# Performance work log

Hardware: AMD Instinct MI355X
Metric: run time of the kernel (lower is better)

## Reference

```python
import jax, jax.numpy as jnp
import numpy as np

E = 768            # bert_embed_dim
D = 3 * E          # LSTM input size = bert_embed_dim * 3
H = 3 * E          # LSTM hidden size = bert_embed_dim * 3
B = 16             # batch
T = 64             # max sequence length


def setup_inputs() -> dict:
    key = jax.random.key(0)
    ks = jax.random.split(key, 12)
    mention_feature = jax.random.normal(ks[0], (B, T, D), jnp.float32)
    start = jax.random.randint(ks[1], (B,), 1, T // 2).astype(jnp.int32)
    end = (start + jax.random.randint(ks[2], (B,), 1, 8)).astype(jnp.int32)
    length = jnp.minimum(end + jax.random.randint(ks[3], (B,), 0, T // 2), T)
    mention_mask = (jnp.arange(T)[None, :] < length[:, None]).astype(jnp.int32)
    s = 0.02
    W_ih = jax.random.normal(ks[4], (4 * H, D), jnp.float32) * s
    W_hh = jax.random.normal(ks[5], (4 * H, H), jnp.float32) * s
    b_ih = jax.random.normal(ks[6], (4 * H,), jnp.float32) * s
    b_hh = jax.random.normal(ks[7], (4 * H,), jnp.float32) * s
    W_out = jax.random.normal(ks[8], (E, 2 * H), jnp.float32) * s
    b_out = jax.random.normal(ks[9], (E,), jnp.float32) * s
    return dict(mention_feature=mention_feature, mention_mask=mention_mask,
                start=start, end=end, W_ih=W_ih, W_hh=W_hh, b_ih=b_ih,
                b_hh=b_hh, W_out=W_out, b_out=b_out)


def lstm_last(seq, lens, W_ih, W_hh, b_ih, b_hh):
    """Masked single-layer LSTM over padded [B,T,D] seqs; returns last valid h [B,H].
    PyTorch gate order: i, f, g, o. State frozen once t >= lens, so the final
    carry equals the output at each sample's last valid timestep."""
    Bb, Tt, _ = seq.shape
    Hh = W_hh.shape[1]
    # precompute input projection for all steps: [B,T,4H]
    xp = jnp.einsum('btd,gd->btg', seq, W_ih) + (b_ih + b_hh)

    def step(carry, inp):
        h, c = carry
        xt, t = inp
        gates = xt + h @ W_hh.T  # [B,4H]
        i_, f_, g_, o_ = jnp.split(gates, 4, axis=-1)
        c_new = jax.nn.sigmoid(f_) * c + jax.nn.sigmoid(i_) * jnp.tanh(g_)
        h_new = jax.nn.sigmoid(o_) * jnp.tanh(c_new)
        upd = (t < lens)[:, None]
        return (jnp.where(upd, h_new, h), jnp.where(upd, c_new, c)), None

    h0 = jnp.zeros((Bb, Hh), seq.dtype)
    (h, _), _ = jax.lax.scan(step, (h0, h0),
                             (xp.transpose(1, 0, 2), jnp.arange(Tt)))
    return h


def reference(mention_feature, mention_mask, start, end,
              W_ih, W_hh, b_ih, b_hh, W_out, b_out):
    Bb, Tt, Dd = mention_feature.shape
    length = jnp.sum(mention_mask, axis=-1)  # [B]

    # left context: tokens [1 : start); if start <= 1 -> single zero step
    left_seq = mention_feature[:, 1:, :]                       # [B,T-1,D]
    tl = jnp.arange(Tt - 1)
    left_valid = tl[None, :] < (start - 1)[:, None]            # [B,T-1]
    left_seq = left_seq * left_valid[..., None]
    left_len = jnp.maximum(start - 1, 1)
    h_left = lstm_last(left_seq, left_len, W_ih, W_hh, b_ih, b_hh)

    # right context: tokens [end : length); if length <= end -> single zero step
    tr = jnp.arange(Tt)
    idx = jnp.clip(end[:, None] + tr[None, :], 0, Tt - 1)      # [B,T]
    right_seq = jnp.take_along_axis(mention_feature, idx[..., None], axis=1)
    right_valid = tr[None, :] < (length - end)[:, None]
    right_seq = right_seq * right_valid[..., None]
    right_len = jnp.maximum(length - end, 1)
    h_right = lstm_last(right_seq, right_len, W_ih, W_hh, b_ih, b_hh)

    feat = jnp.concatenate([h_left, h_right], axis=-1)         # [B,6E]
    return feat @ W_out.T + b_out                              # [B,E]
```

## Files before the change

### kernel.cpp

```cpp
#include <hip/hip_runtime.h>

#define Dd 2304
#define Hh 2304
#define G4 9216
#define TMAX 32
#define NSEQ 32
#define NBLK 192

typedef __bf16 bf16x8 __attribute__((ext_vector_type(8)));
typedef float f32x4 __attribute__((ext_vector_type(4)));
typedef unsigned short u16x8 __attribute__((ext_vector_type(8)));

#define XP_OFF   16384ull
#define WIHB_OFF (XP_OFF  + 1024ull * 9216ull * 4ull)
#define ABF_OFF  (WIHB_OFF + 9216ull * 2304ull * 2ull)
#define HB_OFF   (ABF_OFF + 1024ull * 2304ull * 2ull)
#define FLAG_BASE 2560

static __device__ __forceinline__ unsigned short f2bf(float f) {
  unsigned int u = __float_as_uint(f);
  u += 0x7fffu + ((u >> 16) & 1u);
  return (unsigned short)(u >> 16);
}
static __device__ __forceinline__ float bf2f(unsigned short u) {
  return __uint_as_float(((unsigned int)u) << 16);
}
static __device__ __forceinline__ float sigm(float x) { return 1.0f / (1.0f + expf(-x)); }

static __device__ __forceinline__ void st_h_llc(unsigned short* p, unsigned short v) {
  asm volatile("global_store_short %0, %1, off sc0 sc1"
               :: "v"(p), "v"((unsigned)v) : "memory");
}

__global__ void prep_kernel(const int* __restrict__ mask, const int* __restrict__ start,
                            const int* __restrict__ endp, int* __restrict__ meta) {
  __shared__ int len_s[16];
  const int tid = threadIdx.x;
  for (int i = 2112 + tid; i < 4096; i += 256)
    meta[i] = 0;
  if (tid < 16) {
    int s = 0;
    #pragma unroll 8
    for (int t = 0; t < 64; ++t) s += mask[tid * 64 + t];
    len_s[tid] = s;
  }
  __syncthreads();
  if (tid == 0) {
    int lens[NSEQ]; int ml = 0;
    for (int s = 0; s < NSEQ; ++s) {
      int l;
      if (s < 16) l = start[s] - 1;
      else        l = len_s[s - 16] - endp[s - 16];
      if (l < 1) l = 1;
      if (l > TMAX) l = TMAX;
      lens[s] = l; meta[s] = l; if (l > ml) ml = l;
    }
    meta[32] = ml;
    int* rsrc = meta + 64;
    int* rdst = meta + 64 + 1024;
    int R = 0;
    for (int s = 0; s < NSEQ; ++s) {
      const int b = s & 15;
      const int st = start[b], ln = len_s[b], en = endp[b];
      for (int t = 0; t < lens[s]; ++t) {
        int src = -1;
        if (s < 16) { if (t < st - 1)  src = (b * 64 + t + 1) * Dd; }
        else        { if (t < ln - en) src = (b * 64 + en + t) * Dd; }
        rsrc[R] = src; rdst[R] = s * TMAX + t; ++R;
      }
    }
    meta[33] = R;
    int i = R;
    for (int s = 0; s < NSEQ; ++s)
      for (int t = lens[s]; t < TMAX; ++t) { rsrc[i] = -1; rdst[i] = s * TMAX + t; ++i; }
  }
}

__global__ void cast_wih_kernel(const float4* __restrict__ in, uint2* __restrict__ out) {
  const int i = blockIdx.x * 256 + threadIdx.x;
  const float4 v = in[i];
  uint2 o;
  o.x = (unsigned)f2bf(v.x) | ((unsigned)f2bf(v.y) << 16);
  o.y = (unsigned)f2bf(v.z) | ((unsigned)f2bf(v.w) << 16);
  out[i] = o;
}

__global__ void cast_a_kernel(const float* __restrict__ feat, const int* __restrict__ meta,
                              uint4* __restrict__ abf) {
  const int r = blockIdx.x;
  const int src = meta[64 + r];
  const int tid = threadIdx.x;
  uint4* orow = abf + (size_t)r * 288;
  for (int c = tid; c < 288; c += 256) {
    uint4 o = {0, 0, 0, 0};
    if (src >= 0) {
      const float4 f0 = *(const float4*)(feat + src + c * 8);
      const float4 f1 = *(const float4*)(feat + src + c * 8 + 4);
      o.x = (unsigned)f2bf(f0.x) | ((unsigned)f2bf(f0.y) << 16);
      o.y = (unsigned)f2bf(f0.z) | ((unsigned)f2bf(f0.w) << 16);
      o.z = (unsigned)f2bf(f1.x) | ((unsigned)f2bf(f1.y) << 16);
      o.w = (unsigned)f2bf(f1.z) | ((unsigned)f2bf(f1.w) << 16);
    }
    orow[c] = o;
  }
}

#define LDA 40
__global__ __launch_bounds__(256) void xp_gemm(
    const unsigned short* __restrict__ abf, const unsigned short* __restrict__ wihb,
    const float* __restrict__ bih, const float* __restrict__ bhh,
    const int* __restrict__ meta, float* __restrict__ xp)
{
  const int R = meta[33];
  const int m0 = blockIdx.y * 128;
  if (m0 >= R) return;
  const int n0 = blockIdx.x * 128;
  __shared__ unsigned short As[128 * LDA];
  __shared__ unsigned short Bs[128 * LDA];
  const int tid = threadIdx.x;
  const int srow = tid >> 1;
  const int skk  = (tid & 1) * 16;
  const int* rdst = meta + 64 + 1024;
  const unsigned short* ap = abf  + (size_t)(m0 + srow) * Dd + skk;
  const unsigned short* bp = wihb + (size_t)(n0 + srow) * Dd + skk;

  const int w = tid >> 6, lane = tid & 63;
  const int l16 = lane & 15, quad = lane >> 4;
  const int wm = (w >> 1) * 64, wn = (w & 1) * 64;

  f32x4 acc[4][4] = {};
  for (int kk = 0; kk < Dd; kk += 32) {
    const u16x8 a0 = *(const u16x8*)(ap + kk);
    const u16x8 a1 = *(const u16x8*)(ap + kk + 8);
    const u16x8 b0 = *(const u16x8*)(bp + kk);
    const u16x8 b1 = *(const u16x8*)(bp + kk + 8);
    __syncthreads();
    *(u16x8*)&As[srow * LDA + skk]     = a0;
    *(u16x8*)&As[srow * LDA + skk + 8] = a1;
    *(u16x8*)&Bs[srow * LDA + skk]     = b0;
    *(u16x8*)&Bs[srow * LDA + skk + 8] = b1;
    __syncthreads();
    bf16x8 af[4], bfr[4];
    #pragma unroll
    for (int i = 0; i < 4; ++i) {
      af[i]  = __builtin_bit_cast(bf16x8, *(const u16x8*)&As[(wm + i * 16 + l16) * LDA + quad * 8]);
      bfr[i] = __builtin_bit_cast(bf16x8, *(const u16x8*)&Bs[(wn + i * 16 + l16) * LDA + quad * 8]);
    }
    #pragma unroll
    for (int mi = 0; mi < 4; ++mi)
      #pragma unroll
      for (int ni = 0; ni < 4; ++ni)
        acc[mi][ni] = __builtin_amdgcn_mfma_f32_16x16x32_bf16(af[mi], bfr[ni], acc[mi][ni], 0, 0, 0);
  }
  #pragma unroll
  for (int ni = 0; ni < 4; ++ni) {
    const int col = n0 + wn + ni * 16 + l16;
    const float bsum = bih[col] + bhh[col];
    #pragma unroll
    for (int mi = 0; mi < 4; ++mi)
      #pragma unroll
      for (int r = 0; r < 4; ++r) {
        const int row = m0 + wm + mi * 16 + quad * 4 + r;
        const int dr = rdst[row];
        xp[(size_t)dr * G4 + col] = acc[mi][ni][r] + bsum;
      }
  }
}

__global__ __launch_bounds__(256, 1) void lstm_persist(
    const float* __restrict__ whh, const float* __restrict__ xp,
    int* __restrict__ meta, unsigned short* __restrict__ hb,
    const float* __restrict__ wout, const float* __restrict__ bout,
    float* __restrict__ out)
{
  const int tid = threadIdx.x;
  const int bid = blockIdx.x;
  const int j0 = bid * 12;
  const int w = tid >> 6, lane = tid & 63;
  const int l16 = lane & 15, quad = lane >> 4;
  const int maxlen = meta[32];
  int* flags = meta + FLAG_BASE;
#define HBUF(t) (hb + (size_t)(t) * (NSEQ * Hh))

  __shared__ float red[4][32][49];

  u16x8 Bfr[54];
  #pragma unroll
  for (int n = 0; n < 3; ++n) {
    const int rl = n * 16 + l16;
    const int g = rl / 12, j = rl - g * 12;
    const float* bp = whh + (size_t)(g * Hh + j0 + j) * Hh + w * 576 + quad * 8;
    #pragma unroll
    for (int kf = 0; kf < 18; ++kf) {
      const float4 f0 = *(const float4*)(bp + kf * 32);
      const float4 f1 = *(const float4*)(bp + kf * 32 + 4);
      u16x8 v;
      v[0] = f2bf(f0.x); v[1] = f2bf(f0.y); v[2] = f2bf(f0.z); v[3] = f2bf(f0.w);
      v[4] = f2bf(f1.x); v[5] = f2bf(f1.y); v[6] = f2bf(f1.z); v[7] = f2bf(f1.w);
      Bfr[n * 18 + kf] = v;
    }
  }

  const int sA = tid / 12, jA = tid - sA * 12;
  const int cB = 256 + tid;
  const int sB = cB / 12, jB = cB - sB * 12;
  const int lenA = meta[sA];
  const int lenB = (tid < 128) ? meta[sB] : 0;
  float cstA = 0.f, hvA = 0.f, cstB = 0.f, hvB = 0.f;

  {
    const float* p = xp + (size_t)(sA * TMAX) * G4 + j0 + jA;
    const float vi = p[0], vg = p[2 * Hh], vo = p[3 * Hh];
    cstA = sigm(vi) * tanhf(vg);
    hvA = sigm(vo) * tanhf(cstA);
    st_h_llc(HBUF(1) + sA * Hh + j0 + jA, f2bf(hvA));
    if (tid < 128) {
      const float* q = xp + (size_t)(sB * TMAX) * G4 + j0 + jB;
      const float wi = q[0], wg = q[2 * Hh], wo = q[3 * Hh];
      cstB = sigm(wi) * tanhf(wg);
      hvB = sigm(wo) * tanhf(cstB);
      st_h_llc(HBUF(1) + sB * Hh + j0 + jB, f2bf(hvB));
    }
  }

  float xiA, xfA, xgA, xoA, xiB = 0, xfB = 0, xgB = 0, xoB = 0;
  asm volatile("s_waitcnt vmcnt(0)" ::: "memory");
  __syncthreads();
  if (tid == 0)
    __hip_atomic_store(flags + bid, 1, __ATOMIC_RELAXED, __HIP_MEMORY_SCOPE_AGENT);
  if (1 < maxlen) {
    { const float* p = xp + (size_t)(sA * TMAX + 1) * G4 + j0 + jA;
      xiA = p[0]; xfA = p[Hh]; xgA = p[2 * Hh]; xoA = p[3 * Hh]; }
    if (tid < 128) {
      const float* q = xp + (size_t)(sB * TMAX + 1) * G4 + j0 + jB;
      xiB = q[0]; xfB = q[Hh]; xgB = q[2 * Hh]; xoB = q[3 * Hh];
    }
  }
  if (tid < NBLK) {
    while (__hip_atomic_load(flags + tid, __ATOMIC_RELAXED, __HIP_MEMORY_SCOPE_AGENT) < 1)
      __builtin_amdgcn_s_sleep(2);
  }
  __syncthreads();

  for (int t = 1; t < maxlen; ++t) {
    const unsigned short* hin = HBUF(t);
    unsigned short* hout      = HBUF(t + 1);
    f32x4 acc[2][3] = {};
    const unsigned short* pa = hin + (size_t)l16 * Hh + w * 576 + quad * 8;
    #pragma unroll
    for (int kf = 0; kf < 18; ++kf) {
      const bf16x8 a0 = __builtin_bit_cast(bf16x8, *(const u16x8*)(pa + kf * 32));
      const bf16x8 a1 = __builtin_bit_cast(bf16x8, *(const u16x8*)(pa + kf * 32 + 16 * Hh));
      #pragma unroll
      for (int n = 0; n < 3; ++n) {
        const bf16x8 bv = __builtin_bit_cast(bf16x8, Bfr[n * 18 + kf]);
        acc[0][n] = __builtin_amdgcn_mfma_f32_16x16x32_bf16(a0, bv, acc[0][n], 0, 0, 0);
        acc[1][n] = __builtin_amdgcn_mfma_f32_16x16x32_bf16(a1, bv, acc[1][n], 0, 0, 0);
      }
    }
    #pragma unroll
    for (int m = 0; m < 2; ++m)
      #pragma unroll
      for (int n = 0; n < 3; ++n)
        #pragma unroll
        for (int r = 0; r < 4; ++r)
          red[w][m * 16 + quad * 4 + r][n * 16 + l16] = acc[m][n][r];
    __syncthreads();
    if (t < lenA) {
      const float vi = xiA + red[0][sA][jA]      + red[1][sA][jA]      + red[2][sA][jA]      + red[3][sA][jA];
      const float vf = xfA + red[0][sA][12 + jA] + red[1][sA][12 + jA] + red[2][sA][12 + jA] + red[3][sA][12 + jA];
      const float vg = xgA + red[0][sA][24 + jA] + red[1][sA][24 + jA] + red[2][sA][24 + jA] + red[3][sA][24 + jA];
      const float vo = xoA + red[0][sA][36 + jA] + red[1][sA][36 + jA] + red[2][sA][36 + jA] + red[3][sA][36 + jA];
      cstA = sigm(vf) * cstA + sigm(vi) * tanhf(vg);
      hvA = sigm(vo) * tanhf(cstA);
    }
    st_h_llc(hout + sA * Hh + j0 + jA, f2bf(hvA));
    if (tid < 128) {
      if (t < lenB) {
        const float vi = xiB + red[0][sB][jB]      + red[1][sB][jB]      + red[2][sB][jB]      + red[3][sB][jB];
        const float vf = xfB + red[0][sB][12 + jB] + red[1][sB][12 + jB] + red[2][sB][12 + jB] + red[3][sB][12 + jB];
        const float vg = xgB + red[0][sB][24 + jB] + red[1][sB][24 + jB] + red[2][sB][24 + jB] + red[3][sB][24 + jB];
        const float vo = xoB + red[0][sB][36 + jB] + red[1][sB][36 + jB] + red[2][sB][36 + jB] + red[3][sB][36 + jB];
        cstB = sigm(vf) * cstB + sigm(vi) * tanhf(vg);
        hvB = sigm(vo) * tanhf(cstB);
      }
      st_h_llc(hout + sB * Hh + j0 + jB, f2bf(hvB));
    }
    asm volatile("s_waitcnt vmcnt(0)" ::: "memory");
    __syncthreads();
    if (tid == 0)
      __hip_atomic_store(flags + bid, t + 1, __ATOMIC_RELAXED, __HIP_MEMORY_SCOPE_AGENT);
    if (t + 1 < maxlen) {
      { const float* p = xp + (size_t)(sA * TMAX + t + 1) * G4 + j0 + jA;
        xiA = p[0]; xfA = p[Hh]; xgA = p[2 * Hh]; xoA = p[3 * Hh]; }
      if (tid < 128) {
        const float* q = xp + (size_t)(sB * TMAX + t + 1) * G4 + j0 + jB;
        xiB = q[0]; xfB = q[Hh]; xgB = q[2 * Hh]; xoB = q[3 * Hh];
      }
    }
    if (tid < NBLK) {
      while (__hip_atomic_load(flags + tid, __ATOMIC_RELAXED, __HIP_MEMORY_SCOPE_AGENT) < t + 1)
        __builtin_amdgcn_s_sleep(2);
    }
    __syncthreads();
  }

  const unsigned short* hf = HBUF(maxlen);
  const int o = tid >> 2, p4 = tid & 3;
  const int ee = o & 3, bb = o >> 2;
  const int e = bid * 4 + ee;
  const int hrow = (p4 < 2) ? bb : (16 + bb);
  const int kb = (p4 & 1) * 1152;
  const unsigned short* hp = hf + hrow * Hh + kb;
  const float* wp = wout + (size_t)e * 4608 + p4 * 1152;
  float acco = 0.f;
  #pragma unroll 4
  for (int i = 0; i < 1152; i += 8) {
    const u16x8 hv = *(const u16x8*)(hp + i);
    const float4 w0 = *(const float4*)(wp + i);
    const float4 w1 = *(const float4*)(wp + i + 4);
    acco += bf2f(hv[0]) * w0.x + bf2f(hv[1]) * w0.y + bf2f(hv[2]) * w0.z + bf2f(hv[3]) * w0.w
          + bf2f(hv[4]) * w1.x + bf2f(hv[5]) * w1.y + bf2f(hv[6]) * w1.z + bf2f(hv[7]) * w1.w;
  }
  acco += __shfl_xor(acco, 1);
  acco += __shfl_xor(acco, 2);
  if (p4 == 0) out[bb * 768 + e] = acco + bout[e];
}

extern "C" void kernel_launch(void* const* d_in, const int* in_sizes, int n_in,
                              void* d_out, int out_size, void* d_ws, size_t ws_size,
                              hipStream_t stream)
{
  const float* feat = (const float*)d_in[0];
  const int* mask   = (const int*)d_in[1];
  const int* start  = (const int*)d_in[2];
  const int* endp   = (const int*)d_in[3];
  const float* wih  = (const float*)d_in[4];
  const float* whh  = (const float*)d_in[5];
  const float* bih  = (const float*)d_in[6];
  const float* bhh  = (const float*)d_in[7];
  const float* wout = (const float*)d_in[8];
  const float* bout = (const float*)d_in[9];
  float* out = (float*)d_out;
  char* ws = (char*)d_ws;

  int* meta = (int*)ws;
  float* xp = (float*)(ws + XP_OFF);
  unsigned short* wihb = (unsigned short*)(ws + WIHB_OFF);
  unsigned short* abf  = (unsigned short*)(ws + ABF_OFF);
  unsigned short* hb   = (unsigned short*)(ws + HB_OFF);

  hipLaunchKernelGGL(prep_kernel, dim3(1), dim3(256), 0, stream, mask, start, endp, meta);
  hipLaunchKernelGGL(cast_wih_kernel, dim3(20736), dim3(256), 0, stream,
                     (const float4*)wih, (uint2*)wihb);
  hipLaunchKernelGGL(cast_a_kernel, dim3(1024), dim3(256), 0, stream,
                     feat, meta, (uint4*)abf);
  hipLaunchKernelGGL(xp_gemm, dim3(72, 8), dim3(256), 0, stream,
                     abf, wihb, bih, bhh, meta, xp);
  hipLaunchKernelGGL(lstm_persist, dim3(NBLK), dim3(256), 0, stream,
                     whh, xp, meta, hb, wout, bout, out);
}
```

Baseline: 710.0 us.

## Halve persistent LSTM grid with 512-thread blocks and use direct-to-LDS loads in GEMM

Changes the recurrent LSTM kernel from 192 blocks of 256 threads to 96 blocks of 512 threads. Each block now owns 24 hidden units, split across two wave halves by gate pair, so fewer blocks take part in the per-step grid-wide flag barrier. Flags become fetch-add counters and the spin-wait gets an iteration cap. Separately, the input-projection GEMM loads tiles straight into LDS with global_load_lds and an unpadded layout, which removes the register staging step but may add LDS bank conflicts. The cap on spinning and the doubled register and LDS pressure per block are possible risks.

After: 974.3 us. 1.37x slower.

```diff
diff --git a/kernel.cpp b/kernel.cpp
--- a/kernel.cpp
+++ b/kernel.cpp
@@ -5,7 +5,8 @@
 #define G4 9216
 #define TMAX 32
 #define NSEQ 32
-#define NBLK 192
+#define NBLK 96
+#define SPIN_CAP 100000000u
 
 typedef __bf16 bf16x8 __attribute__((ext_vector_type(8)));
 typedef float f32x4 __attribute__((ext_vector_type(4)));
@@ -30,6 +31,12 @@
 static __device__ __forceinline__ void st_h_llc(unsigned short* p, unsigned short v) {
   asm volatile("global_store_short %0, %1, off sc0 sc1"
                :: "v"(p), "v"((unsigned)v) : "memory");
+}
+
+static __device__ __forceinline__ void gload_lds16(const unsigned short* g, unsigned short* l) {
+  __builtin_amdgcn_global_load_lds(
+      (const __attribute__((address_space(1))) unsigned int*)g,
+      (__attribute__((address_space(3))) unsigned int*)l, 16, 0, 0);
 }
 
 __global__ void prep_kernel(const int* __restrict__ mask, const int* __restrict__ start,
@@ -105,7 +112,6 @@
   }
 }
 
-#define LDA 40
 __global__ __launch_bounds__(256) void xp_gemm(
     const unsigned short* __restrict__ abf, const unsigned short* __restrict__ wihb,
     const float* __restrict__ bih, const float* __restrict__ bhh,
@@ -115,36 +121,38 @@
   const int m0 = blockIdx.y * 128;
   if (m0 >= R) return;
   const int n0 = blockIdx.x * 128;
-  __shared__ unsigned short As[128 * LDA];
-  __shared__ unsigned short Bs[128 * LDA];
+  __shared__ unsigned short As[128 * 32];
+  __shared__ unsigned short Bs[128 * 32];
   const int tid = threadIdx.x;
-  const int srow = tid >> 1;
-  const int skk  = (tid & 1) * 16;
-  const int* rdst = meta + 64 + 1024;
-  const unsigned short* ap = abf  + (size_t)(m0 + srow) * Dd + skk;
-  const unsigned short* bp = wihb + (size_t)(n0 + srow) * Dd + skk;
-
   const int w = tid >> 6, lane = tid & 63;
   const int l16 = lane & 15, quad = lane >> 4;
   const int wm = (w >> 1) * 64, wn = (w & 1) * 64;
+  const int* rdst = meta + 64 + 1024;
+
+  const int rg = lane >> 2;
+  const int kc = (lane & 3) * 8;
+  const unsigned short* gA0 = abf  + (size_t)(m0 + (w * 2 + 0) * 16 + rg) * Dd + kc;
+  const unsigned short* gA1 = abf  + (size_t)(m0 + (w * 2 + 1) * 16 + rg) * Dd + kc;
+  const unsigned short* gB0 = wihb + (size_t)(n0 + (w * 2 + 0) * 16 + rg) * Dd + kc;
+  const unsigned short* gB1 = wihb + (size_t)(n0 + (w * 2 + 1) * 16 + rg) * Dd + kc;
+  unsigned short* lA0 = &As[(w * 2 + 0) * 512];
+  unsigned short* lA1 = &As[(w * 2 + 1) * 512];
+  unsigned short* lB0 = &Bs[(w * 2 + 0) * 512];
+  unsigned short* lB1 = &Bs[(w * 2 + 1) * 512];
 
   f32x4 acc[4][4] = {};
   for (int kk = 0; kk < Dd; kk += 32) {
-    const u16x8 a0 = *(const u16x8*)(ap + kk);
-    const u16x8 a1 = *(const u16x8*)(ap + kk + 8);
-    const u16x8 b0 = *(const u16x8*)(bp + kk);
-    const u16x8 b1 = *(const u16x8*)(bp + kk + 8);
-    __syncthreads();
-    *(u16x8*)&As[srow * LDA + skk]     = a0;
-    *(u16x8*)&As[srow * LDA + skk + 8] = a1;
-    *(u16x8*)&Bs[srow * LDA + skk]     = b0;
-    *(u16x8*)&Bs[srow * LDA + skk + 8] = b1;
+    __syncthreads();
+    gload_lds16(gA0 + kk, lA0);
+    gload_lds16(gA1 + kk, lA1);
+    gload_lds16(gB0 + kk, lB0);
+    gload_lds16(gB1 + kk, lB1);
     __syncthreads();
     bf16x8 af[4], bfr[4];
     #pragma unroll
     for (int i = 0; i < 4; ++i) {
-      af[i]  = __builtin_bit_cast(bf16x8, *(const u16x8*)&As[(wm + i * 16 + l16) * LDA + quad * 8]);
-      bfr[i] = __builtin_bit_cast(bf16x8, *(const u16x8*)&Bs[(wn + i * 16 + l16) * LDA + quad * 8]);
+      af[i]  = __builtin_bit_cast(bf16x8, *(const u16x8*)&As[(wm + i * 16 + l16) * 32 + quad * 8]);
+      bfr[i] = __builtin_bit_cast(bf16x8, *(const u16x8*)&Bs[(wn + i * 16 + l16) * 32 + quad * 8]);
     }
     #pragma unroll
     for (int mi = 0; mi < 4; ++mi)
@@ -167,7 +175,7 @@
   }
 }
 
-__global__ __launch_bounds__(256, 1) void lstm_persist(
+__global__ __launch_bounds__(512, 2) void lstm_persist(
     const float* __restrict__ whh, const float* __restrict__ xp,
     int* __restrict__ meta, unsigned short* __restrict__ hb,
     const float* __restrict__ wout, const float* __restrict__ bout,
@@ -175,21 +183,23 @@
 {
   const int tid = threadIdx.x;
   const int bid = blockIdx.x;
-  const int j0 = bid * 12;
+  const int j0 = bid * 24;
   const int w = tid >> 6, lane = tid & 63;
   const int l16 = lane & 15, quad = lane >> 4;
+  const int kpart = w & 3;
+  const int nh = w >> 2;
   const int maxlen = meta[32];
   int* flags = meta + FLAG_BASE;
 #define HBUF(t) (hb + (size_t)(t) * (NSEQ * Hh))
 
-  __shared__ float red[4][32][49];
+  __shared__ float red[2][4][32][49];
 
   u16x8 Bfr[54];
   #pragma unroll
   for (int n = 0; n < 3; ++n) {
-    const int rl = n * 16 + l16;
-    const int g = rl / 12, j = rl - g * 12;
-    const float* bp = whh + (size_t)(g * Hh + j0 + j) * Hh + w * 576 + quad * 8;
+    const int rl = nh * 48 + n * 16 + l16;
+    const int g = rl / 24, j = rl - g * 24;
+    const float* bp = whh + (size_t)(g * Hh + j0 + j) * Hh + kpart * 576 + quad * 8;
     #pragma unroll
     for (int kf = 0; kf < 18; ++kf) {
       const float4 f0 = *(const float4*)(bp + kf * 32);
@@ -201,11 +211,11 @@
     }
   }
 
-  const int sA = tid / 12, jA = tid - sA * 12;
-  const int cB = 256 + tid;
-  const int sB = cB / 12, jB = cB - sB * 12;
+  const int sA = tid / 24, jA = tid - sA * 24;
+  const int cB = 512 + tid;
+  const int sB = cB / 24, jB = cB - sB * 24;
   const int lenA = meta[sA];
-  const int lenB = (tid < 128) ? meta[sB] : 0;
+  const int lenB = (tid < 256) ? meta[sB] : 0;
   float cstA = 0.f, hvA = 0.f, cstB = 0.f, hvB = 0.f;
 
   {
@@ -214,7 +224,7 @@
     cstA = sigm(vi) * tanhf(vg);
     hvA = sigm(vo) * tanhf(cstA);
     st_h_llc(HBUF(1) + sA * Hh + j0 + jA, f2bf(hvA));
-    if (tid < 128) {
+    if (tid < 256) {
       const float* q = xp + (size_t)(sB * TMAX) * G4 + j0 + jB;
       const float wi = q[0], wg = q[2 * Hh], wo = q[3 * Hh];
       cstB = sigm(wi) * tanhf(wg);
@@ -227,17 +237,19 @@
   asm volatile("s_waitcnt vmcnt(0)" ::: "memory");
   __syncthreads();
   if (tid == 0)
-    __hip_atomic_store(flags + bid, 1, __ATOMIC_RELAXED, __HIP_MEMORY_SCOPE_AGENT);
+    __hip_atomic_fetch_add(flags + bid, 1, __ATOMIC_RELAXED, __HIP_MEMORY_SCOPE_AGENT);
   if (1 < maxlen) {
     { const float* p = xp + (size_t)(sA * TMAX + 1) * G4 + j0 + jA;
       xiA = p[0]; xfA = p[Hh]; xgA = p[2 * Hh]; xoA = p[3 * Hh]; }
-    if (tid < 128) {
+    if (tid < 256) {
       const float* q = xp + (size_t)(sB * TMAX + 1) * G4 + j0 + jB;
       xiB = q[0]; xfB = q[Hh]; xgB = q[2 * Hh]; xoB = q[3 * Hh];
     }
   }
   if (tid < NBLK) {
-    while (__hip_atomic_load(flags + tid, __ATOMIC_RELAXED, __HIP_MEMORY_SCOPE_AGENT) < 1)
+    unsigned spin = 0;
+    while (__hip_atomic_load(flags + tid, __ATOMIC_RELAXED, __HIP_MEMORY_SCOPE_AGENT) < 1 &&
+           ++spin < SPIN_CAP)
       __builtin_amdgcn_s_sleep(2);
   }
   __syncthreads();
@@ -246,7 +258,7 @@
     const unsigned short* hin = HBUF(t);
     unsigned short* hout      = HBUF(t + 1);
     f32x4 acc[2][3] = {};
-    const unsigned short* pa = hin + (size_t)l16 * Hh + w * 576 + quad * 8;
+    const unsigned short* pa = hin + (size_t)l16 * Hh + kpart * 576 + quad * 8;
     #pragma unroll
     for (int kf = 0; kf < 18; ++kf) {
       const bf16x8 a0 = __builtin_bit_cast(bf16x8, *(const u16x8*)(pa + kf * 32));
@@ -264,23 +276,23 @@
       for (int n = 0; n < 3; ++n)
         #pragma unroll
         for (int r = 0; r < 4; ++r)
-          red[w][m * 16 + quad * 4 + r][n * 16 + l16] = acc[m][n][r];
+          red[nh][kpart][m * 16 + quad * 4 + r][n * 16 + l16] = acc[m][n][r];
     __syncthreads();
     if (t < lenA) {
-      const float vi = xiA + red[0][sA][jA]      + red[1][sA][jA]      + red[2][sA][jA]      + red[3][sA][jA];
-      const float vf = xfA + red[0][sA][12 + jA] + red[1][sA][12 + jA] + red[2][sA][12 + jA] + red[3][sA][12 + jA];
-      const float vg = xgA + red[0][sA][24 + jA] + red[1][sA][24 + jA] + red[2][sA][24 + jA] + red[3][sA][24 + jA];
-      const float vo = xoA + red[0][sA][36 + jA] + red[1][sA][36 + jA] + red[2][sA][36 + jA] + red[3][sA][36 + jA];
+      const float vi = xiA + red[0][0][sA][jA]      + red[0][1][sA][jA]      + red[0][2][sA][jA]      + red[0][3][sA][jA];
+      const float vf = xfA + red[0][0][sA][24 + jA] + red[0][1][sA][24 + jA] + red[0][2][sA][24 + jA] + red[0][3][sA][24 + jA];
+      const float vg = xgA + red[1][0][sA][jA]      + red[1][1][sA][jA]      + red[1][2][sA][jA]      + red[1][3][sA][jA];
+      const float vo = xoA + red[1][0][sA][24 + jA] + red[1][1][sA][24 + jA] + red[1][2][sA][24 + jA] + red[1][3][sA][24 + jA];
       cstA = sigm(vf) * cstA + sigm(vi) * tanhf(vg);
       hvA = sigm(vo) * tanhf(cstA);
     }
     st_h_llc(hout + sA * Hh + j0 + jA, f2bf(hvA));
-    if (tid < 128) {
+    if (tid < 256) {
       if (t < lenB) {
-        const float vi = xiB + red[0][sB][jB]      + red[1][sB][jB]      + red[2][sB][jB]      + red[3][sB][jB];
-        const float vf = xfB + red[0][sB][12 + jB] + red[1][sB][12 + jB] + red[2][sB][12 + jB] + red[3][sB][12 + jB];
-        const float vg = xgB + red[0][sB][24 + jB] + red[1][sB][24 + jB] + red[2][sB][24 + jB] + red[3][sB][24 + jB];
-        const float vo = xoB + red[0][sB][36 + jB] + red[1][sB][36 + jB] + red[2][sB][36 + jB] + red[3][sB][36 + jB];
+        const float vi = xiB + red[0][0][sB][jB]      + red[0][1][sB][jB]      + red[0][2][sB][jB]      + red[0][3][sB][jB];
+        const float vf = xfB + red[0][0][sB][24 + jB] + red[0][1][sB][24 + jB] + red[0][2][sB][24 + jB] + red[0][3][sB][24 + jB];
+        const float vg = xgB + red[1][0][sB][jB]      + red[1][1][sB][jB]      + red[1][2][sB][jB]      + red[1][3][sB][jB];
+        const float vo = xoB + red[1][0][sB][24 + jB] + red[1][1][sB][24 + jB] + red[1][2][sB][24 + jB] + red[1][3][sB][24 + jB];
         cstB = sigm(vf) * cstB + sigm(vi) * tanhf(vg);
         hvB = sigm(vo) * tanhf(cstB);
       }
@@ -289,17 +301,19 @@
     asm volatile("s_waitcnt vmcnt(0)" ::: "memory");
     __syncthreads();
     if (tid == 0)
-      __hip_atomic_store(flags + bid, t + 1, __ATOMIC_RELAXED, __HIP_MEMORY_SCOPE_AGENT);
+      __hip_atomic_fetch_add(flags + bid, 1, __ATOMIC_RELAXED, __HIP_MEMORY_SCOPE_AGENT);
     if (t + 1 < maxlen) {
       { const float* p = xp + (size_t)(sA * TMAX + t + 1) * G4 + j0 + jA;
         xiA = p[0]; xfA = p[Hh]; xgA = p[2 * Hh]; xoA = p[3 * Hh]; }
-      if (tid < 128) {
+      if (tid < 256) {
         const float* q = xp + (size_t)(sB * TMAX + t + 1) * G4 + j0 + jB;
         xiB = q[0]; xfB = q[Hh]; xgB = q[2 * Hh]; xoB = q[3 * Hh];
       }
     }
     if (tid < NBLK) {
-      while (__hip_atomic_load(flags + tid, __ATOMIC_RELAXED, __HIP_MEMORY_SCOPE_AGENT) < t + 1)
+      unsigned spin = 0;
+      while (__hip_atomic_load(flags + tid, __ATOMIC_RELAXED, __HIP_MEMORY_SCOPE_AGENT) < t + 1 &&
+             ++spin < SPIN_CAP)
         __builtin_amdgcn_s_sleep(2);
     }
     __syncthreads();
@@ -307,8 +321,8 @@
 
   const unsigned short* hf = HBUF(maxlen);
   const int o = tid >> 2, p4 = tid & 3;
-  const int ee = o & 3, bb = o >> 2;
-  const int e = bid * 4 + ee;
+  const int ee = o & 7, bb = o >> 3;
+  const int e = bid * 8 + ee;
   const int hrow = (p4 < 2) ? bb : (16 + bb);
   const int kb = (p4 & 1) * 1152;
   const unsigned short* hp = hf + hrow * Hh + kb;
@@ -357,6 +371,6 @@
                      feat, meta, (uint4*)abf);
   hipLaunchKernelGGL(xp_gemm, dim3(72, 8), dim3(256), 0, stream,
                      abf, wihb, bih, bhh, meta, xp);
-  hipLaunchKernelGGL(lstm_persist, dim3(NBLK), dim3(256), 0, stream,
+  hipLaunchKernelGGL(lstm_persist, dim3(NBLK), dim3(512), 0, stream,
                      whh, xp, meta, hb, wout, bout, out);
 }
```

## Use direct global-to-LDS loads in xp GEMM and busy-spin grid barrier

Applied to the files above, without the earlier changes.

The xp GEMM tile load now uses global_load_lds to write 16-byte chunks straight into unpadded shared tiles, bypassing registers. The LSTM grid barrier drops s_sleep and instead busy-spins with dummy FMAs, with all 256 threads polling (the extra 64 re-check existing flags) and an iteration cap. The intent is to cut barrier wake-up latency on the per-step critical path and remove register staging in the GEMM. In exchange, the unpadded LDS layout may cause bank conflicts, and the spin cap could silently break synchronization if it is ever reached.

New measurement: 706.4 us. Within noise of the previous version (-0.5%).

```diff
diff --git a/kernel.cpp b/kernel.cpp
--- a/kernel.cpp
+++ b/kernel.cpp
@@ -6,6 +6,7 @@
 #define TMAX 32
 #define NSEQ 32
 #define NBLK 192
+#define SPIN_CAP 100000000u
 
 typedef __bf16 bf16x8 __attribute__((ext_vector_type(8)));
 typedef float f32x4 __attribute__((ext_vector_type(4)));
@@ -30,6 +31,24 @@
 static __device__ __forceinline__ void st_h_llc(unsigned short* p, unsigned short v) {
   asm volatile("global_store_short %0, %1, off sc0 sc1"
                :: "v"(p), "v"((unsigned)v) : "memory");
+}
+
+static __device__ __forceinline__ void gload_lds16(const unsigned short* g, unsigned short* l) {
+  __builtin_amdgcn_global_load_lds(
+      (const __attribute__((address_space(1))) unsigned int*)g,
+      (__attribute__((address_space(3))) unsigned int*)l, 16, 0, 0);
+}
+
+static __device__ __forceinline__ void spin_flag(const int* f, int target) {
+  unsigned spin = 0;
+  float z0 = 1.0f;
+  const float z1 = 1.0000001f;
+  while (__hip_atomic_load(f, __ATOMIC_RELAXED, __HIP_MEMORY_SCOPE_AGENT) < target &&
+         ++spin < SPIN_CAP) {
+    #pragma unroll
+    for (int u = 0; u < 16; ++u) z0 = __builtin_fmaf(z0, z1, 1.0e-30f);
+    asm volatile("" :: "v"(z0));
+  }
 }
 
 __global__ void prep_kernel(const int* __restrict__ mask, const int* __restrict__ start,
@@ -105,7 +124,6 @@
   }
 }
 
-#define LDA 40
 __global__ __launch_bounds__(256) void xp_gemm(
     const unsigned short* __restrict__ abf, const unsigned short* __restrict__ wihb,
     const float* __restrict__ bih, const float* __restrict__ bhh,
@@ -115,36 +133,38 @@
   const int m0 = blockIdx.y * 128;
   if (m0 >= R) return;
   const int n0 = blockIdx.x * 128;
-  __shared__ unsigned short As[128 * LDA];
-  __shared__ unsigned short Bs[128 * LDA];
+  __shared__ unsigned short As[128 * 32];
+  __shared__ unsigned short Bs[128 * 32];
   const int tid = threadIdx.x;
-  const int srow = tid >> 1;
-  const int skk  = (tid & 1) * 16;
-  const int* rdst = meta + 64 + 1024;
-  const unsigned short* ap = abf  + (size_t)(m0 + srow) * Dd + skk;
-  const unsigned short* bp = wihb + (size_t)(n0 + srow) * Dd + skk;
-
   const int w = tid >> 6, lane = tid & 63;
   const int l16 = lane & 15, quad = lane >> 4;
   const int wm = (w >> 1) * 64, wn = (w & 1) * 64;
+  const int* rdst = meta + 64 + 1024;
+
+  const int rg = lane >> 2;
+  const int kc = (lane & 3) * 8;
+  const unsigned short* gA0 = abf  + (size_t)(m0 + (w * 2 + 0) * 16 + rg) * Dd + kc;
+  const unsigned short* gA1 = abf  + (size_t)(m0 + (w * 2 + 1) * 16 + rg) * Dd + kc;
+  const unsigned short* gB0 = wihb + (size_t)(n0 + (w * 2 + 0) * 16 + rg) * Dd + kc;
+  const unsigned short* gB1 = wihb + (size_t)(n0 + (w * 2 + 1) * 16 + rg) * Dd + kc;
+  unsigned short* lA0 = &As[(w * 2 + 0) * 512];
+  unsigned short* lA1 = &As[(w * 2 + 1) * 512];
+  unsigned short* lB0 = &Bs[(w * 2 + 0) * 512];
+  unsigned short* lB1 = &Bs[(w * 2 + 1) * 512];
 
   f32x4 acc[4][4] = {};
   for (int kk = 0; kk < Dd; kk += 32) {
-    const u16x8 a0 = *(const u16x8*)(ap + kk);
-    const u16x8 a1 = *(const u16x8*)(ap + kk + 8);
-    const u16x8 b0 = *(const u16x8*)(bp + kk);
-    const u16x8 b1 = *(const u16x8*)(bp + kk + 8);
-    __syncthreads();
-    *(u16x8*)&As[srow * LDA + skk]     = a0;
-    *(u16x8*)&As[srow * LDA + skk + 8] = a1;
-    *(u16x8*)&Bs[srow * LDA + skk]     = b0;
-    *(u16x8*)&Bs[srow * LDA + skk + 8] = b1;
+    __syncthreads();
+    gload_lds16(gA0 + kk, lA0);
+    gload_lds16(gA1 + kk, lA1);
+    gload_lds16(gB0 + kk, lB0);
+    gload_lds16(gB1 + kk, lB1);
     __syncthreads();
     bf16x8 af[4], bfr[4];
     #pragma unroll
     for (int i = 0; i < 4; ++i) {
-      af[i]  = __builtin_bit_cast(bf16x8, *(const u16x8*)&As[(wm + i * 16 + l16) * LDA + quad * 8]);
-      bfr[i] = __builtin_bit_cast(bf16x8, *(const u16x8*)&Bs[(wn + i * 16 + l16) * LDA + quad * 8]);
+      af[i]  = __builtin_bit_cast(bf16x8, *(const u16x8*)&As[(wm + i * 16 + l16) * 32 + quad * 8]);
+      bfr[i] = __builtin_bit_cast(bf16x8, *(const u16x8*)&Bs[(wn + i * 16 + l16) * 32 + quad * 8]);
     }
     #pragma unroll
     for (int mi = 0; mi < 4; ++mi)
@@ -180,6 +200,7 @@
   const int l16 = lane & 15, quad = lane >> 4;
   const int maxlen = meta[32];
   int* flags = meta + FLAG_BASE;
+  const int fidx = (tid < NBLK) ? tid : (tid - 64);
 #define HBUF(t) (hb + (size_t)(t) * (NSEQ * Hh))
 
   __shared__ float red[4][32][49];
@@ -236,10 +257,7 @@
       xiB = q[0]; xfB = q[Hh]; xgB = q[2 * Hh]; xoB = q[3 * Hh];
     }
   }
-  if (tid < NBLK) {
-    while (__hip_atomic_load(flags + tid, __ATOMIC_RELAXED, __HIP_MEMORY_SCOPE_AGENT) < 1)
-      __builtin_amdgcn_s_sleep(2);
-  }
+  spin_flag(flags + fidx, 1);
   __syncthreads();
 
   for (int t = 1; t < maxlen; ++t) {
@@ -298,10 +316,7 @@
         xiB = q[0]; xfB = q[Hh]; xgB = q[2 * Hh]; xoB = q[3 * Hh];
       }
     }
-    if (tid < NBLK) {
-      while (__hip_atomic_load(flags + tid, __ATOMIC_RELAXED, __HIP_MEMORY_SCOPE_AGENT) < t + 1)
-        __builtin_amdgcn_s_sleep(2);
-    }
+    spin_flag(flags + fidx, t + 1);
     __syncthreads();
   }
 
```
